# Kernel tuning notes

Hardware: AMD Instinct MI355X
Metric: run time of the kernel (lower is better)

Reference implementation:

```python
import jax, jax.numpy as jnp
import numpy as np
from jax import lax

EPS = 1e-5

def _zpool(x):
    # cat(max over channel, mean over channel) -> [B,2,H,W]
    return jnp.concatenate([x.max(axis=1, keepdims=True), x.mean(axis=1, keepdims=True)], axis=1)

def _gate(x, w, g, b, m, v):
    # ZPool -> 7x7 conv (2->1, same pad) -> inference BN -> sigmoid -> scale input
    z = _zpool(x)
    y = lax.conv_general_dilated(z, w, (1, 1), [(3, 3), (3, 3)],
                                 dimension_numbers=('NCHW', 'OIHW', 'NCHW'))
    scale = g / jnp.sqrt(v + EPS)
    y = (y - m[None, :, None, None]) * scale[None, :, None, None] + b[None, :, None, None]
    return x * jax.nn.sigmoid(y)


def setup_inputs() -> dict:
    key = jax.random.key(0)
    ks = jax.random.split(key, 8)
    B, C, H, W = 8, 256, 64, 64
    inp = {
        'x': jax.random.normal(ks[0], (B, C, H, W), dtype=jnp.float32),
        'w_cw': jax.random.normal(ks[1], (1, 2, 7, 7), dtype=jnp.float32) * 0.1,
        'g_cw': jnp.ones((1,), jnp.float32), 'b_cw': jnp.zeros((1,), jnp.float32),
        'm_cw': jnp.zeros((1,), jnp.float32), 'v_cw': jnp.ones((1,), jnp.float32),
        'w_hc': jax.random.normal(ks[2], (1, 2, 7, 7), dtype=jnp.float32) * 0.1,
        'g_hc': jnp.ones((1,), jnp.float32), 'b_hc': jnp.zeros((1,), jnp.float32),
        'm_hc': jnp.zeros((1,), jnp.float32), 'v_hc': jnp.ones((1,), jnp.float32),
        'w_hw': jax.random.normal(ks[3], (1, 2, 7, 7), dtype=jnp.float32) * 0.1,
        'g_hw': jnp.ones((1,), jnp.float32), 'b_hw': jnp.zeros((1,), jnp.float32),
        'm_hw': jnp.zeros((1,), jnp.float32), 'v_hw': jnp.ones((1,), jnp.float32),
        'w1d': jax.random.normal(ks[4], (3, 1, 7), dtype=jnp.float32) * 0.1,
    }
    return inp


def reference(x, w_cw, g_cw, b_cw, m_cw, v_cw,
              w_hc, g_hc, b_hc, m_hc, v_hc,
              w_hw, g_hw, b_hw, m_hw, v_hw, w1d):
    # branch 1: attend over (C) with H as channel dim
    b1 = _gate(x.transpose(0, 2, 1, 3), w_cw, g_cw, b_cw, m_cw, v_cw).transpose(0, 2, 1, 3)
    # branch 2: attend with W as channel dim
    b2 = _gate(x.transpose(0, 3, 2, 1), w_hc, g_hc, b_hc, m_hc, v_hc).transpose(0, 3, 2, 1)
    # branch 3: spatial attention in native layout
    b3 = _gate(x, w_hw, g_hw, b_hw, m_hw, v_hw)

    x_out = (b1 + b2 + b3) / 3.0
    pooled = x_out.mean(axis=(2, 3))                     # [B, C]
    logits = lax.conv_general_dilated(pooled[:, None, :], w1d, (1,), [(3, 3)],
                                      dimension_numbers=('NCH', 'OIH', 'NCH'))  # [B,3,C]
    wts = jax.nn.softmax(logits, axis=1)[..., None, None]  # [B,3,C,1,1]
    branches = jnp.stack([b1, b2, b3], axis=1)             # [B,3,C,H,W]
    return (wts * branches).sum(axis=1)
```

## Files before the change

kernel.cpp:

```cpp
#include <hip/hip_runtime.h>
#include <math.h>

#define BB 8
#define CC 256
#define HH 64
#define WW 64
#define EPS 1e-5f

__global__ __launch_bounds__(256) void pool_hw_kernel(
    const float* __restrict__ x,
    float* __restrict__ z1max, float* __restrict__ z1mean,
    float* __restrict__ z2max, float* __restrict__ z2mean)
{
    int bc = blockIdx.x;
    int b = bc >> 8, c = bc & 255;
    const float* xt = x + (size_t)bc * (HH * WW);

    __shared__ float tile[HH * 65];
    __shared__ float red[512];
    int t = threadIdx.x;

    for (int i = t; i < HH * WW; i += 256) {
        int h = i >> 6, w = i & 63;
        tile[h * 65 + w] = xt[i];
    }
    __syncthreads();

    {
        int w = t & 63, hg = t >> 6;
        float m = -INFINITY, s = 0.f;
        #pragma unroll
        for (int i = 0; i < 16; ++i) {
            float v = tile[(hg * 16 + i) * 65 + w];
            m = fmaxf(m, v); s += v;
        }
        red[t] = m; red[256 + t] = s;
    }
    __syncthreads();
    if (t < 64) {
        int w = t;
        float m = red[w], s = red[256 + w];
        #pragma unroll
        for (int g = 1; g < 4; ++g) { m = fmaxf(m, red[g * 64 + w]); s += red[256 + g * 64 + w]; }
        z1max [bc * WW + w] = m;
        z1mean[bc * WW + w] = s * (1.f / 64.f);
    }
    __syncthreads();

    {
        int h = t & 63, wg = t >> 6;
        float m = -INFINITY, s = 0.f;
        #pragma unroll
        for (int i = 0; i < 16; ++i) {
            float v = tile[h * 65 + wg * 16 + i];
            m = fmaxf(m, v); s += v;
        }
        red[t] = m; red[256 + t] = s;
    }
    __syncthreads();
    if (t < 64) {
        int h = t;
        float m = red[h], s = red[256 + h];
        #pragma unroll
        for (int g = 1; g < 4; ++g) { m = fmaxf(m, red[g * 64 + h]); s += red[256 + g * 64 + h]; }
        z2max [(b * HH + h) * CC + c] = m;
        z2mean[(b * HH + h) * CC + c] = s * (1.f / 64.f);
    }
}

__global__ __launch_bounds__(256) void pool_c_kernel(
    const float* __restrict__ x,
    float* __restrict__ z3max, float* __restrict__ z3mean)
{
    int bh = blockIdx.x;
    int b = bh >> 6, h = bh & 63;
    int t = threadIdx.x;
    int w = t & 63, cg = t >> 6;

    const float* base = x + ((size_t)b * CC * HH + h) * WW + w;
    float m = -INFINITY, s = 0.f;
    #pragma unroll 4
    for (int i = 0; i < 64; ++i) {
        float v = base[(size_t)(cg * 64 + i) * (HH * WW)];
        m = fmaxf(m, v); s += v;
    }
    __shared__ float red[512];
    red[t] = m; red[256 + t] = s;
    __syncthreads();
    if (t < 64) {
        #pragma unroll
        for (int g = 1; g < 4; ++g) { m = fmaxf(m, red[g * 64 + w]); s += red[256 + g * 64 + w]; }
        z3max [bh * WW + w] = m;
        z3mean[bh * WW + w] = s * (1.f / 256.f);
    }
}

__global__ __launch_bounds__(256) void conv_gate_kernel(
    const float* __restrict__ z1max, const float* __restrict__ z1mean,
    const float* __restrict__ w0p, const float* g0, const float* b0,
    const float* m0, const float* v0, float* __restrict__ s1,
    const float* __restrict__ z2max, const float* __restrict__ z2mean,
    const float* __restrict__ w1p, const float* g1, const float* b1,
    const float* m1, const float* v1, float* __restrict__ s2,
    const float* __restrict__ z3max, const float* __restrict__ z3mean,
    const float* __restrict__ w2p, const float* g2, const float* b2,
    const float* m2, const float* v2, float* __restrict__ s3)
{
    int br = blockIdx.y;
    const float *zm, *za, *wp, *gp, *bp, *mp, *vp;
    float* sp; int R, Cw;
    if (br == 0)      { zm=z1max; za=z1mean; wp=w0p; gp=g0; bp=b0; mp=m0; vp=v0; sp=s1; R=CC; Cw=WW; }
    else if (br == 1) { zm=z2max; za=z2mean; wp=w1p; gp=g1; bp=b1; mp=m1; vp=v1; sp=s2; R=HH; Cw=CC; }
    else              { zm=z3max; za=z3mean; wp=w2p; gp=g2; bp=b2; mp=m2; vp=v2; sp=s3; R=HH; Cw=WW; }

    int total = BB * R * Cw;
    int o = blockIdx.x * 256 + threadIdx.x;
    if (o >= total) return;

    int b   = o / (R * Cw);
    int rem = o - b * R * Cw;
    int r   = rem / Cw;
    int col = rem - r * Cw;

    const float* zmb = zm + (size_t)b * R * Cw;
    const float* zab = za + (size_t)b * R * Cw;

    float acc = 0.f;
    #pragma unroll
    for (int dr = 0; dr < 7; ++dr) {
        int rr = r + dr - 3;
        if (rr < 0 || rr >= R) continue;
        #pragma unroll
        for (int dc = 0; dc < 7; ++dc) {
            int cc = col + dc - 3;
            if (cc < 0 || cc >= Cw) continue;
            float wm = wp[dr * 7 + dc];
            float wa = wp[49 + dr * 7 + dc];
            acc += wm * zmb[rr * Cw + cc] + wa * zab[rr * Cw + cc];
        }
    }
    float scale = gp[0] * rsqrtf(vp[0] + EPS);
    float y = (acc - mp[0]) * scale + bp[0];
    sp[o] = 1.f / (1.f + __expf(-y));
}

__global__ __launch_bounds__(256) void pooled_kernel(
    const float* __restrict__ x,
    const float* __restrict__ s1, const float* __restrict__ s2,
    const float* __restrict__ s3, float* __restrict__ pooled)
{
    int bc = blockIdx.x;
    int b = bc >> 8, c = bc & 255;
    int t = threadIdx.x;
    int w = t & 63, hg = t >> 6;

    const float* xt  = x  + (size_t)bc * (HH * WW);
    float s1v        = s1[bc * WW + w];
    const float* s2b = s2 + (size_t)b * HH * CC + c;
    const float* s3b = s3 + (size_t)b * HH * WW + w;

    float acc = 0.f;
    #pragma unroll 4
    for (int i = 0; i < 16; ++i) {
        int h = hg * 16 + i;
        acc += xt[h * WW + w] * (s1v + s2b[h * CC] + s3b[h * WW]);
    }
    #pragma unroll
    for (int off = 32; off >= 1; off >>= 1) acc += __shfl_down(acc, off);
    __shared__ float r[4];
    if ((t & 63) == 0) r[t >> 6] = acc;
    __syncthreads();
    if (t == 0) pooled[bc] = (r[0] + r[1] + r[2] + r[3]) * (1.f / (4096.f * 3.f));
}

__global__ __launch_bounds__(256) void wts_kernel(
    const float* __restrict__ pooled, const float* __restrict__ w1d,
    float* __restrict__ wts)
{
    int o = blockIdx.x * 256 + threadIdx.x;
    if (o >= BB * CC) return;
    int b = o >> 8, c = o & 255;
    const float* p = pooled + b * CC;

    float lg[3];
    #pragma unroll
    for (int k = 0; k < 3; ++k) {
        float a = 0.f;
        #pragma unroll
        for (int j = 0; j < 7; ++j) {
            int cc = c + j - 3;
            if (cc >= 0 && cc < CC) a += w1d[k * 7 + j] * p[cc];
        }
        lg[k] = a;
    }
    float mx = fmaxf(lg[0], fmaxf(lg[1], lg[2]));
    float e0 = __expf(lg[0] - mx), e1 = __expf(lg[1] - mx), e2 = __expf(lg[2] - mx);
    float inv = 1.f / (e0 + e1 + e2);
    wts[(b * 3 + 0) * CC + c] = e0 * inv;
    wts[(b * 3 + 1) * CC + c] = e1 * inv;
    wts[(b * 3 + 2) * CC + c] = e2 * inv;
}

__global__ __launch_bounds__(256) void final_kernel(
    const float* __restrict__ x,
    const float* __restrict__ s1, const float* __restrict__ s2,
    const float* __restrict__ s3, const float* __restrict__ wts,
    float* __restrict__ out)
{
    int i4 = blockIdx.x * 256 + threadIdx.x;
    int w0   = (i4 & 15) * 4;
    int rest = i4 >> 4;
    int h = rest & 63; rest >>= 6;
    int c = rest & 255;
    int b = rest >> 8;

    const float4 x4  = *(const float4*)(x  + (size_t)i4 * 4);
    const float4 s1v = *(const float4*)(s1 + ((size_t)(b * CC + c)) * WW + w0);
    const float  s2v = s2[(b * HH + h) * CC + c];
    const float4 s3v = *(const float4*)(s3 + ((size_t)(b * HH + h)) * WW + w0);
    float k0 = wts[(b * 3 + 0) * CC + c];
    float k1 = wts[(b * 3 + 1) * CC + c];
    float k2 = wts[(b * 3 + 2) * CC + c];

    float4 o;
    o.x = x4.x * (k0 * s1v.x + k1 * s2v + k2 * s3v.x);
    o.y = x4.y * (k0 * s1v.y + k1 * s2v + k2 * s3v.y);
    o.z = x4.z * (k0 * s1v.z + k1 * s2v + k2 * s3v.z);
    o.w = x4.w * (k0 * s1v.w + k1 * s2v + k2 * s3v.w);
    *(float4*)(out + (size_t)i4 * 4) = o;
}

extern "C" void kernel_launch(void* const* d_in, const int* in_sizes, int n_in,
                              void* d_out, int out_size, void* d_ws, size_t ws_size,
                              hipStream_t stream)
{
    const float* x    = (const float*)d_in[0];
    const float* w_cw = (const float*)d_in[1];
    const float* g_cw = (const float*)d_in[2];
    const float* b_cw = (const float*)d_in[3];
    const float* m_cw = (const float*)d_in[4];
    const float* v_cw = (const float*)d_in[5];
    const float* w_hc = (const float*)d_in[6];
    const float* g_hc = (const float*)d_in[7];
    const float* b_hc = (const float*)d_in[8];
    const float* m_hc = (const float*)d_in[9];
    const float* v_hc = (const float*)d_in[10];
    const float* w_hw = (const float*)d_in[11];
    const float* g_hw = (const float*)d_in[12];
    const float* b_hw = (const float*)d_in[13];
    const float* m_hw = (const float*)d_in[14];
    const float* v_hw = (const float*)d_in[15];
    const float* w1d  = (const float*)d_in[16];
    float* out = (float*)d_out;

    float* ws = (float*)d_ws;
    const size_t N1 = (size_t)BB * CC * WW;
    const size_t N2 = (size_t)BB * HH * CC;
    const size_t N3 = (size_t)BB * HH * WW;
    float* z1max  = ws;
    float* z1mean = z1max  + N1;
    float* z2max  = z1mean + N1;
    float* z2mean = z2max  + N2;
    float* z3max  = z2mean + N2;
    float* z3mean = z3max  + N3;
    float* s1     = z3mean + N3;
    float* s2     = s1 + N1;
    float* s3     = s2 + N2;
    float* pooled = s3 + N3;
    float* wts    = pooled + (size_t)BB * CC;

    pool_hw_kernel<<<BB * CC, 256, 0, stream>>>(x, z1max, z1mean, z2max, z2mean);
    pool_c_kernel <<<BB * HH, 256, 0, stream>>>(x, z3max, z3mean);

    conv_gate_kernel<<<dim3((BB * CC * WW + 255) / 256, 3), 256, 0, stream>>>(
        z1max, z1mean, w_cw, g_cw, b_cw, m_cw, v_cw, s1,
        z2max, z2mean, w_hc, g_hc, b_hc, m_hc, v_hc, s2,
        z3max, z3mean, w_hw, g_hw, b_hw, m_hw, v_hw, s3);

    pooled_kernel<<<BB * CC, 256, 0, stream>>>(x, s1, s2, s3, pooled);
    wts_kernel<<<(BB * CC + 255) / 256, 256, 0, stream>>>(pooled, w1d, wts);

    final_kernel<<<(BB * CC * HH * WW / 4 + 255) / 256, 256, 0, stream>>>(
        x, s1, s2, s3, wts, out);
}
```

Baseline: 155.2 us.

## Merge pooling kernels, factor pooled sum via means, fold softmax weights into final

```diff
diff --git a/kernel.cpp b/kernel.cpp
--- a/kernel.cpp
+++ b/kernel.cpp
@@ -7,91 +7,107 @@
 #define WW 64
 #define EPS 1e-5f
 
-__global__ __launch_bounds__(256) void pool_hw_kernel(
+__global__ __launch_bounds__(256) void pool_kernel(
     const float* __restrict__ x,
     float* __restrict__ z1max, float* __restrict__ z1mean,
-    float* __restrict__ z2max, float* __restrict__ z2mean)
-{
-    int bc = blockIdx.x;
-    int b = bc >> 8, c = bc & 255;
-    const float* xt = x + (size_t)bc * (HH * WW);
-
-    __shared__ float tile[HH * 65];
-    __shared__ float red[512];
+    float* __restrict__ z2max, float* __restrict__ z2mean,
+    float* __restrict__ z3max, float* __restrict__ z3mean)
+{
+    __shared__ float smem[HH * 65 + 512];
+    int blk = blockIdx.x;
     int t = threadIdx.x;
 
-    for (int i = t; i < HH * WW; i += 256) {
-        int h = i >> 6, w = i & 63;
-        tile[h * 65 + w] = xt[i];
-    }
-    __syncthreads();
-
-    {
-        int w = t & 63, hg = t >> 6;
-        float m = -INFINITY, s = 0.f;
+    if (blk < BB * CC) {
+        int bc = blk;
+        int b = bc >> 8, c = bc & 255;
+        const float4* xt4 = (const float4*)x + (size_t)bc * 1024;
+        float* tile = smem;
+        float* red  = smem + HH * 65;
+
         #pragma unroll
+        for (int i = 0; i < 4; ++i) {
+            int idx = t + i * 256;
+            float4 v = xt4[idx];
+            int h = idx >> 4, w0 = (idx & 15) * 4;
+            float* d = &tile[h * 65 + w0];
+            d[0] = v.x; d[1] = v.y; d[2] = v.z; d[3] = v.w;
+        }
+        __syncthreads();
+
+        {
+            int w = t & 63, hg = t >> 6;
+            float m = -INFINITY, s = 0.f;
+            #pragma unroll
+            for (int i = 0; i < 16; ++i) {
+                float v = tile[(hg * 16 + i) * 65 + w];
+                m = fmaxf(m, v); s += v;
+            }
+            red[t] = m; red[256 + t] = s;
+        }
+        __syncthreads();
+        if (t < 64) {
+            int w = t;
+            float m = red[w], s = red[256 + w];
+            #pragma unroll
+            for (int g = 1; g < 4; ++g) { m = fmaxf(m, red[g * 64 + w]); s += red[256 + g * 64 + w]; }
+            z1max [bc * WW + w] = m;
+            z1mean[bc * WW + w] = s * (1.f / 64.f);
+        }
+        __syncthreads();
+
+        {
+            int h = t & 63, wg = t >> 6;
+            float m = -INFINITY, s = 0.f;
+            #pragma unroll
+            for (int i = 0; i < 16; ++i) {
+                float v = tile[h * 65 + wg * 16 + i];
+                m = fmaxf(m, v); s += v;
+            }
+            red[t] = m; red[256 + t] = s;
+        }
+        __syncthreads();
+        if (t < 64) {
+            int h = t;
+            float m = red[h], s = red[256 + h];
+            #pragma unroll
+            for (int g = 1; g < 4; ++g) { m = fmaxf(m, red[g * 64 + h]); s += red[256 + g * 64 + h]; }
+            z2max [(b * HH + h) * CC + c] = m;
+            z2mean[(b * HH + h) * CC + c] = s * (1.f / 64.f);
+        }
+    } else {
+        int bh = blk - BB * CC;
+        int b = bh >> 6, h = bh & 63;
+        int wq = t & 15, cg = t >> 4;
+
+        const float4* base = (const float4*)x
+            + ((size_t)b * CC * HH * WW + (size_t)h * WW) / 4 + wq;
+        float4 m = make_float4(-INFINITY, -INFINITY, -INFINITY, -INFINITY);
+        float4 s = make_float4(0.f, 0.f, 0.f, 0.f);
+        #pragma unroll 4
         for (int i = 0; i < 16; ++i) {
-            float v = tile[(hg * 16 + i) * 65 + w];
-            m = fmaxf(m, v); s += v;
-        }
-        red[t] = m; red[256 + t] = s;
-    }
-    __syncthreads();
-    if (t < 64) {
-        int w = t;
-        float m = red[w], s = red[256 + w];
-        #pragma unroll
-        for (int g = 1; g < 4; ++g) { m = fmaxf(m, red[g * 64 + w]); s += red[256 + g * 64 + w]; }
-        z1max [bc * WW + w] = m;
-        z1mean[bc * WW + w] = s * (1.f / 64.f);
-    }
-    __syncthreads();
-
-    {
-        int h = t & 63, wg = t >> 6;
-        float m = -INFINITY, s = 0.f;
-        #pragma unroll
-        for (int i = 0; i < 16; ++i) {
-            float v = tile[h * 65 + wg * 16 + i];
-            m = fmaxf(m, v); s += v;
-        }
-        red[t] = m; red[256 + t] = s;
-    }
-    __syncthreads();
-    if (t < 64) {
-        int h = t;
-        float m = red[h], s = red[256 + h];
-        #pragma unroll
-        for (int g = 1; g < 4; ++g) { m = fmaxf(m, red[g * 64 + h]); s += red[256 + g * 64 + h]; }
-        z2max [(b * HH + h) * CC + c] = m;
-        z2mean[(b * HH + h) * CC + c] = s * (1.f / 64.f);
-    }
-}
-
-__global__ __launch_bounds__(256) void pool_c_kernel(
-    const float* __restrict__ x,
-    float* __restrict__ z3max, float* __restrict__ z3mean)
-{
-    int bh = blockIdx.x;
-    int b = bh >> 6, h = bh & 63;
-    int t = threadIdx.x;
-    int w = t & 63, cg = t >> 6;
-
-    const float* base = x + ((size_t)b * CC * HH + h) * WW + w;
-    float m = -INFINITY, s = 0.f;
-    #pragma unroll 4
-    for (int i = 0; i < 64; ++i) {
-        float v = base[(size_t)(cg * 64 + i) * (HH * WW)];
-        m = fmaxf(m, v); s += v;
-    }
-    __shared__ float red[512];
-    red[t] = m; red[256 + t] = s;
-    __syncthreads();
-    if (t < 64) {
-        #pragma unroll
-        for (int g = 1; g < 4; ++g) { m = fmaxf(m, red[g * 64 + w]); s += red[256 + g * 64 + w]; }
-        z3max [bh * WW + w] = m;
-        z3mean[bh * WW + w] = s * (1.f / 256.f);
+            float4 v = base[(size_t)(cg * 16 + i) * 1024];
+            m.x = fmaxf(m.x, v.x); m.y = fmaxf(m.y, v.y);
+            m.z = fmaxf(m.z, v.z); m.w = fmaxf(m.w, v.w);
+            s.x += v.x; s.y += v.y; s.z += v.z; s.w += v.w;
+        }
+        float4* mred = (float4*)smem;
+        float4* sred = (float4*)smem + 256;
+        mred[t] = m; sred[t] = s;
+        __syncthreads();
+        if (t < 16) {
+            float4 mm = mred[t], ss = sred[t];
+            #pragma unroll
+            for (int g = 1; g < 16; ++g) {
+                float4 mv = mred[g * 16 + t], sv = sred[g * 16 + t];
+                mm.x = fmaxf(mm.x, mv.x); mm.y = fmaxf(mm.y, mv.y);
+                mm.z = fmaxf(mm.z, mv.z); mm.w = fmaxf(mm.w, mv.w);
+                ss.x += sv.x; ss.y += sv.y; ss.z += sv.z; ss.w += sv.w;
+            }
+            ss.x *= (1.f / 256.f); ss.y *= (1.f / 256.f);
+            ss.z *= (1.f / 256.f); ss.w *= (1.f / 256.f);
+            *(float4*)(z3max  + bh * WW + t * 4) = mm;
+            *(float4*)(z3mean + bh * WW + t * 4) = ss;
+        }
     }
 }
 
@@ -146,24 +162,31 @@
 
 __global__ __launch_bounds__(256) void pooled_kernel(
     const float* __restrict__ x,
-    const float* __restrict__ s1, const float* __restrict__ s2,
+    const float* __restrict__ s1, const float* __restrict__ z1mean,
+    const float* __restrict__ s2, const float* __restrict__ z2mean,
     const float* __restrict__ s3, float* __restrict__ pooled)
 {
     int bc = blockIdx.x;
     int b = bc >> 8, c = bc & 255;
     int t = threadIdx.x;
-    int w = t & 63, hg = t >> 6;
-
-    const float* xt  = x  + (size_t)bc * (HH * WW);
-    float s1v        = s1[bc * WW + w];
-    const float* s2b = s2 + (size_t)b * HH * CC + c;
-    const float* s3b = s3 + (size_t)b * HH * WW + w;
+
+    const float4* xt4 = (const float4*)x  + (size_t)bc * 1024;
+    const float4* s34 = (const float4*)s3 + (size_t)b * 1024;
 
     float acc = 0.f;
-    #pragma unroll 4
-    for (int i = 0; i < 16; ++i) {
-        int h = hg * 16 + i;
-        acc += xt[h * WW + w] * (s1v + s2b[h * CC] + s3b[h * WW]);
+    #pragma unroll
+    for (int i = 0; i < 4; ++i) {
+        float4 xv = xt4[t + i * 256];
+        float4 sv = s34[t + i * 256];
+        acc += xv.x * sv.x + xv.y * sv.y + xv.z * sv.z + xv.w * sv.w;
+    }
+    if (t < 64) {
+        int w = t;
+        acc += 64.f * s1[bc * WW + w] * z1mean[bc * WW + w];
+    } else if (t < 128) {
+        int h = t - 64;
+        int idx = (b * HH + h) * CC + c;
+        acc += 64.f * s2[idx] * z2mean[idx];
     }
     #pragma unroll
     for (int off = 32; off >= 1; off >>= 1) acc += __shfl_down(acc, off);
@@ -173,39 +196,11 @@
     if (t == 0) pooled[bc] = (r[0] + r[1] + r[2] + r[3]) * (1.f / (4096.f * 3.f));
 }
 
-__global__ __launch_bounds__(256) void wts_kernel(
-    const float* __restrict__ pooled, const float* __restrict__ w1d,
-    float* __restrict__ wts)
-{
-    int o = blockIdx.x * 256 + threadIdx.x;
-    if (o >= BB * CC) return;
-    int b = o >> 8, c = o & 255;
-    const float* p = pooled + b * CC;
-
-    float lg[3];
-    #pragma unroll
-    for (int k = 0; k < 3; ++k) {
-        float a = 0.f;
-        #pragma unroll
-        for (int j = 0; j < 7; ++j) {
-            int cc = c + j - 3;
-            if (cc >= 0 && cc < CC) a += w1d[k * 7 + j] * p[cc];
-        }
-        lg[k] = a;
-    }
-    float mx = fmaxf(lg[0], fmaxf(lg[1], lg[2]));
-    float e0 = __expf(lg[0] - mx), e1 = __expf(lg[1] - mx), e2 = __expf(lg[2] - mx);
-    float inv = 1.f / (e0 + e1 + e2);
-    wts[(b * 3 + 0) * CC + c] = e0 * inv;
-    wts[(b * 3 + 1) * CC + c] = e1 * inv;
-    wts[(b * 3 + 2) * CC + c] = e2 * inv;
-}
-
 __global__ __launch_bounds__(256) void final_kernel(
     const float* __restrict__ x,
     const float* __restrict__ s1, const float* __restrict__ s2,
-    const float* __restrict__ s3, const float* __restrict__ wts,
-    float* __restrict__ out)
+    const float* __restrict__ s3, const float* __restrict__ pooled,
+    const float* __restrict__ w1d, float* __restrict__ out)
 {
     int i4 = blockIdx.x * 256 + threadIdx.x;
     int w0   = (i4 & 15) * 4;
@@ -214,13 +209,24 @@
     int c = rest & 255;
     int b = rest >> 8;
 
+    float lg0 = 0.f, lg1 = 0.f, lg2 = 0.f;
+    #pragma unroll
+    for (int j = 0; j < 7; ++j) {
+        int cc = c + j - 3;
+        float p = (cc >= 0 && cc < CC) ? pooled[b * CC + cc] : 0.f;
+        lg0 += w1d[j] * p;
+        lg1 += w1d[7 + j] * p;
+        lg2 += w1d[14 + j] * p;
+    }
+    float mx = fmaxf(lg0, fmaxf(lg1, lg2));
+    float e0 = __expf(lg0 - mx), e1 = __expf(lg1 - mx), e2 = __expf(lg2 - mx);
+    float inv = 1.f / (e0 + e1 + e2);
+    float k0 = e0 * inv, k1 = e1 * inv, k2 = e2 * inv;
+
     const float4 x4  = *(const float4*)(x  + (size_t)i4 * 4);
     const float4 s1v = *(const float4*)(s1 + ((size_t)(b * CC + c)) * WW + w0);
     const float  s2v = s2[(b * HH + h) * CC + c];
     const float4 s3v = *(const float4*)(s3 + ((size_t)(b * HH + h)) * WW + w0);
-    float k0 = wts[(b * 3 + 0) * CC + c];
-    float k1 = wts[(b * 3 + 1) * CC + c];
-    float k2 = wts[(b * 3 + 2) * CC + c];
 
     float4 o;
     o.x = x4.x * (k0 * s1v.x + k1 * s2v + k2 * s3v.x);
@@ -267,19 +273,18 @@
     float* s2     = s1 + N1;
     float* s3     = s2 + N2;
     float* pooled = s3 + N3;
-    float* wts    = pooled + (size_t)BB * CC;
-
-    pool_hw_kernel<<<BB * CC, 256, 0, stream>>>(x, z1max, z1mean, z2max, z2mean);
-    pool_c_kernel <<<BB * HH, 256, 0, stream>>>(x, z3max, z3mean);
+
+    pool_kernel<<<BB * CC + BB * HH, 256, 0, stream>>>(
+        x, z1max, z1mean, z2max, z2mean, z3max, z3mean);
 
     conv_gate_kernel<<<dim3((BB * CC * WW + 255) / 256, 3), 256, 0, stream>>>(
         z1max, z1mean, w_cw, g_cw, b_cw, m_cw, v_cw, s1,
         z2max, z2mean, w_hc, g_hc, b_hc, m_hc, v_hc, s2,
         z3max, z3mean, w_hw, g_hw, b_hw, m_hw, v_hw, s3);
 
-    pooled_kernel<<<BB * CC, 256, 0, stream>>>(x, s1, s2, s3, pooled);
-    wts_kernel<<<(BB * CC + 255) / 256, 256, 0, stream>>>(pooled, w1d, wts);
-
-    final_kernel<<<(BB * CC * HH * WW / 4 + 255) / 256, 256, 0, stream>>>(
-        x, s1, s2, s3, wts, out);
-}
+    pooled_kernel<<<BB * CC, 256, 0, stream>>>(
+        x, s1, z1mean, s2, z2mean, s3, pooled);
+
+    final_kernel<<<(BB * CC * HH * WW / 4) / 256, 256, 0, stream>>>(
+        x, s1, s2, s3, pooled, w1d, out);
+}
```

After: 150.5 us. 1.03x faster.
